# Kernel optimization log

Measured on AMD Instinct MI355X. Metric: run time of the kernel, lower is better.

The kernel has to match this reference:

```python
import jax, jax.numpy as jnp
from jax import lax
import numpy as np

K = 10            # size_feat
N_MU = 10         # number of mean-PSF components
NCH = K * K + N_MU  # 110 depthwise channels
KLEN = 65         # precomputed kernel length


def setup_inputs() -> dict:
    key = jax.random.key(0)
    ks = jax.random.split(key, 12)
    B, C, H, W = 1, 3, 256, 256
    img = jax.random.uniform(ks[0], (B, C, H, W), jnp.float32)
    zernike = jax.random.normal(ks[1], (B, H, W, 35), jnp.float32)
    # pos displacements (first 2 channels) scaled to a few pixels
    zernike = zernike.at[..., :2].multiply(2.0)
    fc1_w = jax.random.normal(ks[2], (200, 33), jnp.float32) / np.float32(np.sqrt(33))
    fc1_b = jax.random.normal(ks[3], (200,), jnp.float32) * 0.01
    fc2_w = jax.random.normal(ks[4], (200, 200), jnp.float32) / np.float32(np.sqrt(200))
    fc2_b = jax.random.normal(ks[5], (200,), jnp.float32) * 0.01
    fc3_w = jax.random.normal(ks[6], (100, 200), jnp.float32) * 0.01
    fc3_b = jnp.zeros((100,), jnp.float32)
    basis_left = jax.random.normal(ks[7], (KLEN, K), jnp.float32) * 0.05
    basis_right = jax.random.normal(ks[8], (KLEN, K), jnp.float32) * 0.05
    mu = jax.random.uniform(ks[9], (KLEN, N_MU), jnp.float32) / np.float32(KLEN)
    return dict(img=img, zernike=zernike, fc1_w=fc1_w, fc1_b=fc1_b,
                fc2_w=fc2_w, fc2_b=fc2_b, fc3_w=fc3_w, fc3_b=fc3_b,
                basis_left=basis_left, basis_right=basis_right, mu=mu, ksize=65)


def _grid_sample_border(img, pos):
    """Bilinear grid_sample, padding_mode='border', align_corners=False.
    img: (B,C,H,W), pos: (B,H,W,2) pixel displacements (x,y)."""
    B, C, H, W = img.shape
    yy, xx = jnp.meshgrid(jnp.arange(H, dtype=jnp.float32),
                          jnp.arange(W, dtype=jnp.float32), indexing='ij')
    grid = jnp.stack((xx, yy), -1)                       # (H,W,2)
    wh = jnp.array([W - 1, H - 1], jnp.float32)
    flow = 2.0 * (grid[None] + pos) / wh - 1.0           # (B,H,W,2) in [-1,1]
    ix = ((flow[..., 0] + 1.0) * W - 1.0) * 0.5
    iy = ((flow[..., 1] + 1.0) * H - 1.0) * 0.5
    ix = jnp.clip(ix, 0.0, W - 1)
    iy = jnp.clip(iy, 0.0, H - 1)
    x0 = jnp.floor(ix); y0 = jnp.floor(iy)
    wx = ix - x0;       wy = iy - y0
    x0i = jnp.clip(x0.astype(jnp.int32), 0, W - 1)
    y0i = jnp.clip(y0.astype(jnp.int32), 0, H - 1)
    x1i = jnp.clip(x0i + 1, 0, W - 1)
    y1i = jnp.clip(y0i + 1, 0, H - 1)

    def bilerp(im, x0i, x1i, y0i, y1i, wx, wy):
        g = lambda yi, xi: im[:, yi, xi]                 # (C,H,W)
        top = g(y0i, x0i) * (1 - wx) + g(y0i, x1i) * wx
        bot = g(y1i, x0i) * (1 - wx) + g(y1i, x1i) * wx
        return top * (1 - wy) + bot * wy

    return jax.vmap(bilerp)(img, x0i, x1i, y0i, y1i, wx, wy)


def _depthwise(x, w, pad_axis, pad):
    # x: (N, NCH, H, W); w: (NCH,1,kh,kw). Reflect 'same' padding on pad_axis.
    cfg = [(0, 0)] * 4
    cfg[pad_axis] = (pad, pad)
    xp = jnp.pad(x, cfg, mode='reflect')
    return lax.conv_general_dilated(
        xp, w, (1, 1), 'VALID',
        dimension_numbers=('NCHW', 'OIHW', 'NCHW'),
        feature_group_count=x.shape[1])


def _forward(img, zernike, fc1_w, fc1_b, fc2_w, fc2_b, fc3_w, fc3_b,
             basis_left, basis_right, mu, ksize):
    B, C, H, W = img.shape
    pad = ksize // 2
    # --- grid-sample warp ---
    tilt = _grid_sample_border(img, zernike[..., :2])    # (B,C,H,W)
    # --- per-pixel MLP -> PSF coefficients ---
    f = zernike[..., 2:]                                  # (B,H,W,33)
    h = jax.nn.leaky_relu(f @ fc1_w.T + fc1_b)
    h = jax.nn.leaky_relu(h @ fc2_w.T + fc2_b)
    coef = h @ fc3_w.T + fc3_b                            # (B,H,W,100)
    weight = jnp.concatenate(
        [coef, jnp.ones((B, H, W, N_MU), coef.dtype)], -1)  # (B,H,W,110)
    # --- elementwise weight multiply ---
    big = jnp.concatenate([tilt, jnp.ones_like(tilt)], 1)  # (B,2C,H,W)
    big = big[..., None] * weight[:, None]                 # (B,2C,H,W,110)
    x = big.reshape(B * 2 * C, H, W, NCH).transpose(0, 3, 1, 2)  # (B*2C,110,H,W)
    # --- separable depthwise blur kernels (outer products Z_i x X_j + mu) ---
    wl = jnp.concatenate([jnp.repeat(basis_left.T, K, axis=0), mu.T], 0)  # (110,klen)
    wr = jnp.concatenate([jnp.tile(basis_right.T, (K, 1)), mu.T], 0)      # (110,klen)
    wl = wl[:, None, :, None]                              # (110,1,klen,1)
    wr = wr[:, None, None, :]                              # (110,1,1,klen)
    y = _depthwise(x, wl, 2, pad)
    y = _depthwise(y, wr, 3, pad)
    d = y.reshape(B, 2 * C, NCH, H, W)
    out = jnp.sum(d[:, :3], axis=2) / jnp.sum(d[:, 3:], axis=2)  # (B,3,H,W)
    return out


def reference(img, zernike, fc1_w, fc1_b, fc2_w, fc2_b, fc3_w, fc3_b,
              basis_left, basis_right, mu, ksize):
    return _forward(img, zernike, fc1_w, fc1_b, fc2_w, fc2_b, fc3_w, fc3_b,
                    basis_left, basis_right, mu, ksize)
```

## Files before the change

### kernel.cpp

```cpp
#include <hip/hip_runtime.h>

#define HW 65536

typedef __attribute__((ext_vector_type(8))) short short8;
typedef __attribute__((ext_vector_type(4))) float float4v;

__device__ __forceinline__ int refl(int i){ if (i < 0) i = -i; if (i > 255) i = 510 - i; return i; }
__device__ __forceinline__ float lrelu(float x){ return x > 0.f ? x : 0.01f * x; }
__device__ __forceinline__ unsigned int f2bf(float x){
  union { float f; unsigned int u; } v; v.f = x;
  unsigned int r = v.u + 0x7fff + ((v.u >> 16) & 1);
  return r >> 16;
}

__global__ __launch_bounds__(256) void k_gridsample(const float* __restrict__ img,
                                                    const float* __restrict__ zern,
                                                    float* __restrict__ tilt){
  int x = threadIdx.x, y = blockIdx.x;
  int pix = y * 256 + x;
  float px = zern[pix * 35 + 0], py = zern[pix * 35 + 1];
  float ix = ((float)x + px) * (256.f / 255.f) - 0.5f;
  float iy = ((float)y + py) * (256.f / 255.f) - 0.5f;
  ix = fminf(fmaxf(ix, 0.f), 255.f);
  iy = fminf(fmaxf(iy, 0.f), 255.f);
  float x0f = floorf(ix), y0f = floorf(iy);
  float wx = ix - x0f, wy = iy - y0f;
  int x0 = (int)x0f, y0 = (int)y0f;
  int x1 = min(x0 + 1, 255), y1 = min(y0 + 1, 255);
  #pragma unroll
  for (int c = 0; c < 3; ++c){
    const float* im = img + c * HW;
    float g00 = im[y0 * 256 + x0], g01 = im[y0 * 256 + x1];
    float g10 = im[y1 * 256 + x0], g11 = im[y1 * 256 + x1];
    float top = g00 * (1.f - wx) + g01 * wx;
    float bot = g10 * (1.f - wx) + g11 * wx;
    tilt[c * HW + pix] = top * (1.f - wy) + bot * wy;
  }
}

#define W2OFF 13312
#define W3OFF 59904
__global__ __launch_bounds__(256) void k_prep(const float* __restrict__ w1,
    const float* __restrict__ w2, const float* __restrict__ w3,
    const float* __restrict__ bl, const float* __restrict__ br,
    const float* __restrict__ mu, unsigned short* __restrict__ wbf,
    unsigned short* __restrict__ Tt){
  int i = blockIdx.x * 256 + threadIdx.x;
  if (i < 84992){
    if (i < 208 * 64){
      int n = i >> 6, k = i & 63;
      float v = (n < 200 && k < 33) ? w1[n * 33 + k] : 0.f;
      wbf[i] = (unsigned short)f2bf(v);
    } else if (i < W2OFF + 208 * 224){
      int j = i - W2OFF; int n = j / 224, k = j - n * 224;
      float v = (n < 200 && k < 200) ? w2[n * 200 + k] : 0.f;
      wbf[i] = (unsigned short)f2bf(v);
    } else {
      int j = i - W3OFF; int n = j / 224, k = j - n * 224;
      float v = (n < 100 && k < 200) ? w3[n * 200 + k] : 0.f;
      wbf[i] = (unsigned short)f2bf(v);
    }
  } else {
    int e = i - 84992;
    int t = e / 1536, rem = e - t * 1536;
    int m = rem / 96, k = rem - m * 96;
    int d = k - m;
    float v = 0.f;
    if (d >= 0 && d <= 64){
      if (t < 10)      v = bl[d * 10 + t];
      else if (t < 20) v = mu[d * 10 + (t - 10)];
      else             v = br[d * 10 + (t - 20)];
    }
    Tt[e] = (unsigned short)f2bf(v);
  }
}

#define HSTR 232
__global__ __launch_bounds__(256) void k_mlp(const float* __restrict__ zern,
    const float* __restrict__ b1f, const float* __restrict__ b2f,
    const float* __restrict__ b3f, const unsigned short* __restrict__ wbf,
    float* __restrict__ coefp){
  __shared__ char smem[29696];
  unsigned short* H1 = (unsigned short*)smem;
  float*          H3 = (float*)smem;
  unsigned short* XB = (unsigned short*)(smem + 14848);
  unsigned short* H2 = XB;
  int tid = threadIdx.x;
  int pix0 = blockIdx.x * 32;
  int lane = tid & 63, wv = tid >> 6;
  int ln = lane & 15, qd = lane >> 4;

  for (int e = tid; e < 1152; e += 256) ((int*)XB)[e] = 0;
  for (int e = tid; e < 384; e += 256){
    int m = e / 12, j = e - m * 12;
    ((int*)H1)[m * 116 + 104 + j] = 0;
  }
  __syncthreads();
  for (int e = tid; e < 32 * 33; e += 256){
    int m = e / 33, k = e - m * 33;
    XB[m * 72 + k] = (unsigned short)f2bf(zern[(pix0 + m) * 35 + 2 + k]);
  }
  __syncthreads();

  for (int nt = wv; nt < 13; nt += 4){
    int n = nt * 16 + ln;
    short8 b0 = *(const short8*)(wbf + n * 64 + qd * 8);
    short8 b1 = *(const short8*)(wbf + n * 64 + 32 + qd * 8);
    float bv = (n < 200) ? b1f[n] : 0.f;
    #pragma unroll
    for (int mt = 0; mt < 2; ++mt){
      float4v acc = {bv, bv, bv, bv};
      short8 a0 = *(const short8*)(XB + (mt * 16 + ln) * 72 + qd * 8);
      short8 a1 = *(const short8*)(XB + (mt * 16 + ln) * 72 + 32 + qd * 8);
      acc = __builtin_amdgcn_mfma_f32_16x16x32_bf16(a0, b0, acc, 0, 0, 0);
      acc = __builtin_amdgcn_mfma_f32_16x16x32_bf16(a1, b1, acc, 0, 0, 0);
      #pragma unroll
      for (int r = 0; r < 4; ++r)
        H1[(mt * 16 + qd * 4 + r) * HSTR + n] = (unsigned short)f2bf(lrelu(acc[r]));
    }
  }
  __syncthreads();

  for (int e = tid; e < 384; e += 256){
    int m = e / 12, j = e - m * 12;
    ((int*)H2)[m * 116 + 104 + j] = 0;
  }
  {
    const unsigned short* w2p = wbf + W2OFF;
    for (int nt = wv; nt < 13; nt += 4){
      int n = nt * 16 + ln;
      short8 bf[7];
      #pragma unroll
      for (int kc = 0; kc < 7; ++kc)
        bf[kc] = *(const short8*)(w2p + n * 224 + kc * 32 + qd * 8);
      float bv = (n < 200) ? b2f[n] : 0.f;
      #pragma unroll
      for (int mt = 0; mt < 2; ++mt){
        float4v acc = {bv, bv, bv, bv};
        #pragma unroll
        for (int kc = 0; kc < 7; ++kc){
          short8 af = *(const short8*)(H1 + (mt * 16 + ln) * HSTR + kc * 32 + qd * 8);
          acc = __builtin_amdgcn_mfma_f32_16x16x32_bf16(af, bf[kc], acc, 0, 0, 0);
        }
        #pragma unroll
        for (int r = 0; r < 4; ++r)
          H2[(mt * 16 + qd * 4 + r) * HSTR + n] = (unsigned short)f2bf(lrelu(acc[r]));
      }
    }
  }
  __syncthreads();

  {
    const unsigned short* w3p = wbf + W3OFF;
    for (int nt = wv; nt < 7; nt += 4){
      int n = nt * 16 + ln;
      short8 bf[7];
      #pragma unroll
      for (int kc = 0; kc < 7; ++kc)
        bf[kc] = *(const short8*)(w3p + n * 224 + kc * 32 + qd * 8);
      float bv = (n < 100) ? b3f[n] : 0.f;
      #pragma unroll
      for (int mt = 0; mt < 2; ++mt){
        float4v acc = {bv, bv, bv, bv};
        #pragma unroll
        for (int kc = 0; kc < 7; ++kc){
          short8 af = *(const short8*)(H2 + (mt * 16 + ln) * HSTR + kc * 32 + qd * 8);
          acc = __builtin_amdgcn_mfma_f32_16x16x32_bf16(af, bf[kc], acc, 0, 0, 0);
        }
        #pragma unroll
        for (int r = 0; r < 4; ++r)
          H3[(mt * 16 + qd * 4 + r) * 113 + n] = acc[r];
      }
    }
  }
  __syncthreads();

  for (int e = tid; e < 3200; e += 256){
    int n = e >> 5, m = e & 31;
    coefp[n * HW + pix0 + m] = H3[m * 113 + n];
  }
}

#define VB 344
__global__ __launch_bounds__(256) void k_vconv13(const float* __restrict__ tilt,
    const float* __restrict__ coefp, const unsigned short* __restrict__ Tt,
    float* __restrict__ sbuf, float* __restrict__ smu){
  __shared__ __align__(16) unsigned short sxb[2][16 * VB];
  int tid = threadIdx.x;
  int bid = blockIdx.x;
  int lane = tid & 63, wv = tid >> 6;
  int ln = lane & 15, qd = lane >> 4;
  int col = tid & 15, seg = tid >> 4;
  int r0 = seg * 20;

  int goff[20];
  #pragma unroll
  for (int q = 0; q < 20; ++q) goff[q] = refl(r0 + q - 32) * 256 + col;

  for (int e = tid; e < 768; e += 256){
    int b = e / 384, r = e - b * 384;
    int cc = r / 24, rp = r - cc * 24;
    sxb[b][cc * VB + 320 + rp] = 0;
  }

  if (bid < 640){
    int s = bid & 15;
    int cj = bid >> 4;
    int c = cj / 10, j = cj - c * 10;
    int x0 = s * 16;
    float treg[20];
    if (c < 3){
      const float* tc = tilt + c * HW + x0;
      #pragma unroll
      for (int q = 0; q < 20; ++q) treg[q] = tc[goff[q]];
    }
    float pf[20];
    {
      const float* cq = coefp + j * HW + x0;
      #pragma unroll
      for (int q = 0; q < 20; ++q) pf[q] = cq[goff[q]];
    }
    float4v acc[4];
    #pragma unroll
    for (int t = 0; t < 4; ++t) acc[t] = (float4v){0.f, 0.f, 0.f, 0.f};
    for (int i = 0; i < 10; ++i){
      int us = i & 1;
      unsigned short* sb = sxb[us];
      #pragma unroll
      for (int q = 0; q < 10; ++q){
        float v0 = pf[2 * q], v1 = pf[2 * q + 1];
        if (c < 3){ v0 *= treg[2 * q]; v1 *= treg[2 * q + 1]; }
        *(unsigned int*)&sb[col * VB + r0 + 2 * q] = f2bf(v0) | (f2bf(v1) << 16);
      }
      __syncthreads();
      if (i < 9){
        const float* cn = coefp + ((i + 1) * 10 + j) * HW + x0;
        #pragma unroll
        for (int q = 0; q < 20; ++q) pf[q] = cn[goff[q]];
      }
      const unsigned short* ta = Tt + i * 1536 + ln * 96 + qd * 8;
      short8 A0 = *(const short8*)(ta);
      short8 A1 = *(const short8*)(ta + 32);
      short8 A2 = *(const short8*)(ta + 64);
      #pragma unroll
      for (int t = 0; t < 4; ++t){
        int yt = wv * 4 + t;
        const unsigned short* bp = sb + ln * VB + yt * 16 + qd * 8;
        short8 B0 = *(const short8*)(bp);
        short8 B1 = *(const short8*)(bp + 32);
        short8 B2 = *(const short8*)(bp + 64);
        acc[t] = __builtin_amdgcn_mfma_f32_16x16x32_bf16(A0, B0, acc[t], 0, 0, 0);
        acc[t] = __builtin_amdgcn_mfma_f32_16x16x32_bf16(A1, B1, acc[t], 0, 0, 0);
        acc[t] = __builtin_amdgcn_mfma_f32_16x16x32_bf16(A2, B2, acc[t], 0, 0, 0);
      }
    }
    float* S = sbuf + (c * 10 + j) * HW + x0 + ln;
    #pragma unroll
    for (int t = 0; t < 4; ++t){
      int yt = wv * 4 + t;
      #pragma unroll
      for (int r = 0; r < 4; ++r)
        S[(yt * 16 + qd * 4 + r) * 256] = acc[t][r];
    }
  } else {
    int b2 = bid - 640;
    int c = b2 >> 4, s = b2 & 15;
    int x0 = s * 16;
    const float* tc = tilt + c * HW + x0;
    float tv[20];
    #pragma unroll
    for (int q = 0; q < 20; ++q) tv[q] = tc[goff[q]];
    #pragma unroll
    for (int q = 0; q < 10; ++q){
      *(unsigned int*)&sxb[0][col * VB + r0 + 2 * q] = f2bf(tv[2 * q]) | (f2bf(tv[2 * q + 1]) << 16);
    }
    __syncthreads();
    for (int m = 0; m < 10; ++m){
      const unsigned short* ta = Tt + (10 + m) * 1536 + ln * 96 + qd * 8;
      short8 A0 = *(const short8*)(ta);
      short8 A1 = *(const short8*)(ta + 32);
      short8 A2 = *(const short8*)(ta + 64);
      float4v acc[4];
      #pragma unroll
      for (int t = 0; t < 4; ++t) acc[t] = (float4v){0.f, 0.f, 0.f, 0.f};
      #pragma unroll
      for (int t = 0; t < 4; ++t){
        int yt = wv * 4 + t;
        const unsigned short* bp = sxb[0] + ln * VB + yt * 16 + qd * 8;
        short8 B0 = *(const short8*)(bp);
        short8 B1 = *(const short8*)(bp + 32);
        short8 B2 = *(const short8*)(bp + 64);
        acc[t] = __builtin_amdgcn_mfma_f32_16x16x32_bf16(A0, B0, acc[t], 0, 0, 0);
        acc[t] = __builtin_amdgcn_mfma_f32_16x16x32_bf16(A1, B1, acc[t], 0, 0, 0);
        acc[t] = __builtin_amdgcn_mfma_f32_16x16x32_bf16(A2, B2, acc[t], 0, 0, 0);
      }
      float* S = smu + (c * 10 + m) * HW + x0 + ln;
      #pragma unroll
      for (int t = 0; t < 4; ++t){
        int yt = wv * 4 + t;
        #pragma unroll
        for (int r = 0; r < 4; ++r)
          S[(yt * 16 + qd * 4 + r) * 256] = acc[t][r];
      }
    }
  }
}

#define HS2 344
__global__ __launch_bounds__(256) void k_hconv8(const float* __restrict__ sbuf,
    const float* __restrict__ smu, const unsigned short* __restrict__ Tt,
    float* __restrict__ part){
  __shared__ __align__(16) unsigned short sxb[16 * HS2];
  int tid = threadIdx.x;
  int grp = blockIdx.x >> 4;
  int yt  = blockIdx.x & 15;
  int y0 = yt * 16;
  int lane = tid & 63, wv = tid >> 6;
  int ln = lane & 15, qd = lane >> 4;
  int srow = tid >> 4, scol = tid & 15;
  int isbr = (grp < 8);
  int tgt, h;
  if (isbr){ tgt = grp >> 1; h = grp & 1; }
  else     { int g2 = grp - 8; tgt = g2 >> 1; h = g2 & 1; }
  const float* base = isbr ? (sbuf + tgt * 10 * HW) : (smu + tgt * 10 * HW);
  int tbase = isbr ? 20 : 10;

  for (int e = tid; e < 384; e += 256){
    int rr = e / 24, cp = e - rr * 24;
    sxb[rr * HS2 + 320 + cp] = 0;
  }

  int gx[20];
  #pragma unroll
  for (int q = 0; q < 20; ++q) gx[q] = refl(scol * 20 - 32 + q);

  float4v acc[4];
  #pragma unroll
  for (int t = 0; t < 4; ++t) acc[t] = (float4v){0.f, 0.f, 0.f, 0.f};

  for (int p = 0; p < 5; ++p){
    int col = h * 5 + p;
    const float* plane = base + col * HW + (y0 + srow) * 256;
    __syncthreads();
    float v[20];
    #pragma unroll
    for (int q = 0; q < 20; ++q) v[q] = plane[gx[q]];
    #pragma unroll
    for (int q = 0; q < 10; ++q){
      *(unsigned int*)&sxb[srow * HS2 + scol * 20 + 2 * q] =
          f2bf(v[2 * q]) | (f2bf(v[2 * q + 1]) << 16);
    }
    __syncthreads();
    const unsigned short* ta = Tt + (tbase + col) * 1536 + ln * 96 + qd * 8;
    short8 A0 = *(const short8*)(ta);
    short8 A1 = *(const short8*)(ta + 32);
    short8 A2 = *(const short8*)(ta + 64);
    #pragma unroll
    for (int t = 0; t < 4; ++t){
      int wt = wv * 4 + t;
      const unsigned short* bp = sxb + ln * HS2 + wt * 16 + qd * 8;
      short8 B0 = *(const short8*)(bp);
      short8 B1 = *(const short8*)(bp + 32);
      short8 B2 = *(const short8*)(bp + 64);
      acc[t] = __builtin_amdgcn_mfma_f32_16x16x32_bf16(A0, B0, acc[t], 0, 0, 0);
      acc[t] = __builtin_amdgcn_mfma_f32_16x16x32_bf16(A1, B1, acc[t], 0, 0, 0);
      acc[t] = __builtin_amdgcn_mfma_f32_16x16x32_bf16(A2, B2, acc[t], 0, 0, 0);
    }
  }
  #pragma unroll
  for (int t = 0; t < 4; ++t){
    int wt = wv * 4 + t;
    float4 res = {acc[t][0], acc[t][1], acc[t][2], acc[t][3]};
    *(float4*)(part + grp * HW + (y0 + ln) * 256 + wt * 16 + qd * 4) = res;
  }
}

__global__ __launch_bounds__(256) void k_final(const float* __restrict__ part,
                                               const float* __restrict__ mu,
                                               float* __restrict__ out){
  int pix = blockIdx.x * 256 + threadIdx.x;
  float muC = 0.f;
  #pragma unroll
  for (int m = 0; m < 10; ++m){
    float s = 0.f;
    for (int u = 0; u < 65; ++u) s += mu[u * 10 + m];
    muC += s * s;
  }
  float den = part[6 * HW + pix] + part[7 * HW + pix] + muC;
  float inv = 1.f / den;
  #pragma unroll
  for (int c = 0; c < 3; ++c){
    float num = part[(2 * c) * HW + pix] + part[(2 * c + 1) * HW + pix]
              + part[(8 + 2 * c) * HW + pix] + part[(9 + 2 * c) * HW + pix];
    out[c * HW + pix] = num * inv;
  }
}

extern "C" void kernel_launch(void* const* d_in, const int* in_sizes, int n_in,
                              void* d_out, int out_size, void* d_ws, size_t ws_size,
                              hipStream_t stream) {
  const float* img  = (const float*)d_in[0];
  const float* zern = (const float*)d_in[1];
  const float* w1   = (const float*)d_in[2];
  const float* b1   = (const float*)d_in[3];
  const float* w2   = (const float*)d_in[4];
  const float* b2   = (const float*)d_in[5];
  const float* w3   = (const float*)d_in[6];
  const float* b3   = (const float*)d_in[7];
  const float* bl   = (const float*)d_in[8];
  const float* br   = (const float*)d_in[9];
  const float* mu   = (const float*)d_in[10];
  float* out = (float*)d_out;

  float* w     = (float*)d_ws;
  float* tilt  = w;
  float* coefp = w + 3 * HW;
  float* part  = w + 3 * HW;
  float* sbuf  = w + 103 * HW;
  float* smu   = w + 143 * HW;
  unsigned short* wbf = (unsigned short*)sbuf;
  unsigned short* Tt  = (unsigned short*)(w + 173 * HW);

  k_gridsample<<<256, 256, 0, stream>>>(img, zern, tilt);
  k_prep<<<512, 256, 0, stream>>>(w1, w2, w3, bl, br, mu, wbf, Tt);
  k_mlp<<<2048, 256, 0, stream>>>(zern, b1, b2, b3, wbf, coefp);
  k_vconv13<<<688, 256, 0, stream>>>(tilt, coefp, Tt, sbuf, smu);
  k_hconv8<<<224, 256, 0, stream>>>(sbuf, smu, Tt, part);
  k_final<<<256, 256, 0, stream>>>(part, mu, out);
}
```

Before: 168.4 us.

## Store vertical-conv intermediates as bf16, merge gridsample/prep kernels, precompute mu constant

The vertical-convolution kernel now writes its intermediate planes (sbuf, smu) as bf16 rather than fp32. The horizontal kernel already converted these values to bf16 before its MFMA, so this halves intermediate memory traffic and removes that conversion. Grid sampling, weight prep and the mu-sum constant are merged into one launch, which drops a kernel launch and stops k_final from recomputing the mu sum in every thread. The extra rounding happens at the same point as before, so numerics should be nearly unchanged.

```diff
diff --git a/kernel.cpp b/kernel.cpp
--- a/kernel.cpp
+++ b/kernel.cpp
@@ -13,65 +13,84 @@
   return r >> 16;
 }
 
-__global__ __launch_bounds__(256) void k_gridsample(const float* __restrict__ img,
-                                                    const float* __restrict__ zern,
-                                                    float* __restrict__ tilt){
-  int x = threadIdx.x, y = blockIdx.x;
-  int pix = y * 256 + x;
-  float px = zern[pix * 35 + 0], py = zern[pix * 35 + 1];
-  float ix = ((float)x + px) * (256.f / 255.f) - 0.5f;
-  float iy = ((float)y + py) * (256.f / 255.f) - 0.5f;
-  ix = fminf(fmaxf(ix, 0.f), 255.f);
-  iy = fminf(fmaxf(iy, 0.f), 255.f);
-  float x0f = floorf(ix), y0f = floorf(iy);
-  float wx = ix - x0f, wy = iy - y0f;
-  int x0 = (int)x0f, y0 = (int)y0f;
-  int x1 = min(x0 + 1, 255), y1 = min(y0 + 1, 255);
-  #pragma unroll
-  for (int c = 0; c < 3; ++c){
-    const float* im = img + c * HW;
-    float g00 = im[y0 * 256 + x0], g01 = im[y0 * 256 + x1];
-    float g10 = im[y1 * 256 + x0], g11 = im[y1 * 256 + x1];
-    float top = g00 * (1.f - wx) + g01 * wx;
-    float bot = g10 * (1.f - wx) + g11 * wx;
-    tilt[c * HW + pix] = top * (1.f - wy) + bot * wy;
-  }
-}
-
 #define W2OFF 13312
 #define W3OFF 59904
-__global__ __launch_bounds__(256) void k_prep(const float* __restrict__ w1,
-    const float* __restrict__ w2, const float* __restrict__ w3,
-    const float* __restrict__ bl, const float* __restrict__ br,
-    const float* __restrict__ mu, unsigned short* __restrict__ wbf,
-    unsigned short* __restrict__ Tt){
-  int i = blockIdx.x * 256 + threadIdx.x;
-  if (i < 84992){
-    if (i < 208 * 64){
-      int n = i >> 6, k = i & 63;
-      float v = (n < 200 && k < 33) ? w1[n * 33 + k] : 0.f;
-      wbf[i] = (unsigned short)f2bf(v);
-    } else if (i < W2OFF + 208 * 224){
-      int j = i - W2OFF; int n = j / 224, k = j - n * 224;
-      float v = (n < 200 && k < 200) ? w2[n * 200 + k] : 0.f;
-      wbf[i] = (unsigned short)f2bf(v);
+__global__ __launch_bounds__(256) void k_gsprep(const float* __restrict__ img,
+    const float* __restrict__ zern,
+    const float* __restrict__ w1, const float* __restrict__ w2,
+    const float* __restrict__ w3, const float* __restrict__ bl,
+    const float* __restrict__ br, const float* __restrict__ mu,
+    float* __restrict__ tilt, unsigned short* __restrict__ wbf,
+    unsigned short* __restrict__ Tt, float* __restrict__ mucp){
+  __shared__ float sm[650];
+  __shared__ float sq[10];
+  int bid = blockIdx.x;
+  int tid = threadIdx.x;
+  if (bid < 256){
+    int x = tid, y = bid;
+    int pix = y * 256 + x;
+    float px = zern[pix * 35 + 0], py = zern[pix * 35 + 1];
+    float ix = ((float)x + px) * (256.f / 255.f) - 0.5f;
+    float iy = ((float)y + py) * (256.f / 255.f) - 0.5f;
+    ix = fminf(fmaxf(ix, 0.f), 255.f);
+    iy = fminf(fmaxf(iy, 0.f), 255.f);
+    float x0f = floorf(ix), y0f = floorf(iy);
+    float wx = ix - x0f, wy = iy - y0f;
+    int x0 = (int)x0f, y0 = (int)y0f;
+    int x1 = min(x0 + 1, 255), y1 = min(y0 + 1, 255);
+    #pragma unroll
+    for (int c = 0; c < 3; ++c){
+      const float* im = img + c * HW;
+      float g00 = im[y0 * 256 + x0], g01 = im[y0 * 256 + x1];
+      float g10 = im[y1 * 256 + x0], g11 = im[y1 * 256 + x1];
+      float top = g00 * (1.f - wx) + g01 * wx;
+      float bot = g10 * (1.f - wx) + g11 * wx;
+      tilt[c * HW + pix] = top * (1.f - wy) + bot * wy;
+    }
+  } else if (bid < 768){
+    int i = (bid - 256) * 256 + tid;
+    if (i < 84992){
+      if (i < 208 * 64){
+        int n = i >> 6, k = i & 63;
+        float v = (n < 200 && k < 33) ? w1[n * 33 + k] : 0.f;
+        wbf[i] = (unsigned short)f2bf(v);
+      } else if (i < W2OFF + 208 * 224){
+        int j = i - W2OFF; int n = j / 224, k = j - n * 224;
+        float v = (n < 200 && k < 200) ? w2[n * 200 + k] : 0.f;
+        wbf[i] = (unsigned short)f2bf(v);
+      } else {
+        int j = i - W3OFF; int n = j / 224, k = j - n * 224;
+        float v = (n < 100 && k < 200) ? w3[n * 200 + k] : 0.f;
+        wbf[i] = (unsigned short)f2bf(v);
+      }
     } else {
-      int j = i - W3OFF; int n = j / 224, k = j - n * 224;
-      float v = (n < 100 && k < 200) ? w3[n * 200 + k] : 0.f;
-      wbf[i] = (unsigned short)f2bf(v);
+      int e = i - 84992;
+      int t = e / 1536, rem = e - t * 1536;
+      int m = rem / 96, k = rem - m * 96;
+      int d = k - m;
+      float v = 0.f;
+      if (d >= 0 && d <= 64){
+        if (t < 10)      v = bl[d * 10 + t];
+        else if (t < 20) v = mu[d * 10 + (t - 10)];
+        else             v = br[d * 10 + (t - 20)];
+      }
+      Tt[e] = (unsigned short)f2bf(v);
     }
   } else {
-    int e = i - 84992;
-    int t = e / 1536, rem = e - t * 1536;
-    int m = rem / 96, k = rem - m * 96;
-    int d = k - m;
-    float v = 0.f;
-    if (d >= 0 && d <= 64){
-      if (t < 10)      v = bl[d * 10 + t];
-      else if (t < 20) v = mu[d * 10 + (t - 10)];
-      else             v = br[d * 10 + (t - 20)];
-    }
-    Tt[e] = (unsigned short)f2bf(v);
+    for (int e = tid; e < 650; e += 256) sm[e] = mu[e];
+    __syncthreads();
+    if (tid < 10){
+      float s = 0.f;
+      for (int u = 0; u < 65; ++u) s += sm[u * 10 + tid];
+      sq[tid] = s * s;
+    }
+    __syncthreads();
+    if (tid == 0){
+      float m = 0.f;
+      #pragma unroll
+      for (int mm = 0; mm < 10; ++mm) m += sq[mm];
+      mucp[0] = m;
+    }
   }
 }
 
@@ -182,9 +201,9 @@
 }
 
 #define VB 344
-__global__ __launch_bounds__(256) void k_vconv13(const float* __restrict__ tilt,
+__global__ __launch_bounds__(256) void k_vconv14(const float* __restrict__ tilt,
     const float* __restrict__ coefp, const unsigned short* __restrict__ Tt,
-    float* __restrict__ sbuf, float* __restrict__ smu){
+    unsigned short* __restrict__ sbuf, unsigned short* __restrict__ smu){
   __shared__ __align__(16) unsigned short sxb[2][16 * VB];
   int tid = threadIdx.x;
   int bid = blockIdx.x;
@@ -254,13 +273,13 @@
         acc[t] = __builtin_amdgcn_mfma_f32_16x16x32_bf16(A2, B2, acc[t], 0, 0, 0);
       }
     }
-    float* S = sbuf + (c * 10 + j) * HW + x0 + ln;
+    unsigned short* S = sbuf + (c * 10 + j) * HW + x0 + ln;
     #pragma unroll
     for (int t = 0; t < 4; ++t){
       int yt = wv * 4 + t;
       #pragma unroll
       for (int r = 0; r < 4; ++r)
-        S[(yt * 16 + qd * 4 + r) * 256] = acc[t][r];
+        S[(yt * 16 + qd * 4 + r) * 256] = (unsigned short)f2bf(acc[t][r]);
     }
   } else {
     int b2 = bid - 640;
@@ -294,21 +313,21 @@
         acc[t] = __builtin_amdgcn_mfma_f32_16x16x32_bf16(A1, B1, acc[t], 0, 0, 0);
         acc[t] = __builtin_amdgcn_mfma_f32_16x16x32_bf16(A2, B2, acc[t], 0, 0, 0);
       }
-      float* S = smu + (c * 10 + m) * HW + x0 + ln;
+      unsigned short* S = smu + (c * 10 + m) * HW + x0 + ln;
       #pragma unroll
       for (int t = 0; t < 4; ++t){
         int yt = wv * 4 + t;
         #pragma unroll
         for (int r = 0; r < 4; ++r)
-          S[(yt * 16 + qd * 4 + r) * 256] = acc[t][r];
+          S[(yt * 16 + qd * 4 + r) * 256] = (unsigned short)f2bf(acc[t][r]);
       }
     }
   }
 }
 
 #define HS2 344
-__global__ __launch_bounds__(256) void k_hconv8(const float* __restrict__ sbuf,
-    const float* __restrict__ smu, const unsigned short* __restrict__ Tt,
+__global__ __launch_bounds__(256) void k_hconv9(const unsigned short* __restrict__ sbuf,
+    const unsigned short* __restrict__ smu, const unsigned short* __restrict__ Tt,
     float* __restrict__ part){
   __shared__ __align__(16) unsigned short sxb[16 * HS2];
   int tid = threadIdx.x;
@@ -322,7 +341,7 @@
   int tgt, h;
   if (isbr){ tgt = grp >> 1; h = grp & 1; }
   else     { int g2 = grp - 8; tgt = g2 >> 1; h = g2 & 1; }
-  const float* base = isbr ? (sbuf + tgt * 10 * HW) : (smu + tgt * 10 * HW);
+  const unsigned short* base = isbr ? (sbuf + tgt * 10 * HW) : (smu + tgt * 10 * HW);
   int tbase = isbr ? 20 : 10;
 
   for (int e = tid; e < 384; e += 256){
@@ -340,15 +359,15 @@
 
   for (int p = 0; p < 5; ++p){
     int col = h * 5 + p;
-    const float* plane = base + col * HW + (y0 + srow) * 256;
+    const unsigned short* plane = base + col * HW + (y0 + srow) * 256;
     __syncthreads();
-    float v[20];
+    unsigned short v[20];
     #pragma unroll
     for (int q = 0; q < 20; ++q) v[q] = plane[gx[q]];
     #pragma unroll
     for (int q = 0; q < 10; ++q){
       *(unsigned int*)&sxb[srow * HS2 + scol * 20 + 2 * q] =
-          f2bf(v[2 * q]) | (f2bf(v[2 * q + 1]) << 16);
+          (unsigned int)v[2 * q] | ((unsigned int)v[2 * q + 1] << 16);
     }
     __syncthreads();
     const unsigned short* ta = Tt + (tbase + col) * 1536 + ln * 96 + qd * 8;
@@ -376,16 +395,10 @@
 }
 
 __global__ __launch_bounds__(256) void k_final(const float* __restrict__ part,
-                                               const float* __restrict__ mu,
+                                               const float* __restrict__ mucp,
                                                float* __restrict__ out){
   int pix = blockIdx.x * 256 + threadIdx.x;
-  float muC = 0.f;
-  #pragma unroll
-  for (int m = 0; m < 10; ++m){
-    float s = 0.f;
-    for (int u = 0; u < 65; ++u) s += mu[u * 10 + m];
-    muC += s * s;
-  }
+  float muC = mucp[0];
   float den = part[6 * HW + pix] + part[7 * HW + pix] + muC;
   float inv = 1.f / den;
   #pragma unroll
@@ -416,15 +429,15 @@
   float* tilt  = w;
   float* coefp = w + 3 * HW;
   float* part  = w + 3 * HW;
-  float* sbuf  = w + 103 * HW;
-  float* smu   = w + 143 * HW;
-  unsigned short* wbf = (unsigned short*)sbuf;
-  unsigned short* Tt  = (unsigned short*)(w + 173 * HW);
-
-  k_gridsample<<<256, 256, 0, stream>>>(img, zern, tilt);
-  k_prep<<<512, 256, 0, stream>>>(w1, w2, w3, bl, br, mu, wbf, Tt);
+  unsigned short* sbuf = (unsigned short*)(w + 103 * HW);
+  unsigned short* smu  = (unsigned short*)(w + 143 * HW);
+  unsigned short* wbf  = (unsigned short*)(w + 103 * HW);
+  unsigned short* Tt   = (unsigned short*)(w + 173 * HW);
+  float* mucp = (float*)(Tt + 46080);
+
+  k_gsprep<<<769, 256, 0, stream>>>(img, zern, w1, w2, w3, bl, br, mu, tilt, wbf, Tt, mucp);
   k_mlp<<<2048, 256, 0, stream>>>(zern, b1, b2, b3, wbf, coefp);
-  k_vconv13<<<688, 256, 0, stream>>>(tilt, coefp, Tt, sbuf, smu);
-  k_hconv8<<<224, 256, 0, stream>>>(sbuf, smu, Tt, part);
-  k_final<<<256, 256, 0, stream>>>(part, mu, out);
-}
+  k_vconv14<<<688, 256, 0, stream>>>(tilt, coefp, Tt, sbuf, smu);
+  k_hconv9<<<224, 256, 0, stream>>>(sbuf, smu, Tt, part);
+  k_final<<<256, 256, 0, stream>>>(part, mucp, out);
+}
```

Result: faster. 156.8 us (-6.9%).
